# Optimization experiments

Hardware: AMD Instinct MI355X
Metric: run time of the kernel (lower is better)

## Reference

```python
import jax, jax.numpy as jnp
import numpy as np

# ---- config (matches init_kwargs) ----
B, C_IN, L, T = 32, 12, 1024, 64
C1, C2, K = 64, 128, 7
PAD = K // 2
NUM_CLASSES = 4
GAIN = 2.0
TH1, TH2 = 0.5, 0.5
TAU1, TAU2 = 1.0, 0.9
RESET = 0.0


def setup_inputs() -> dict:
    key = jax.random.key(0)
    ks = jax.random.split(key, 7)
    x = jax.random.normal(ks[0], (B, C_IN, L, T), dtype=jnp.float32)
    w1 = jax.random.normal(ks[1], (C1, C_IN, K), dtype=jnp.float32) * 0.1
    b1 = jax.random.normal(ks[2], (C1,), dtype=jnp.float32) * 0.01
    w2 = jax.random.normal(ks[3], (C2, C1, K), dtype=jnp.float32) * 0.05
    b2 = jax.random.normal(ks[4], (C2,), dtype=jnp.float32) * 0.01
    fc_w = jax.random.normal(ks[5], (NUM_CLASSES, C2), dtype=jnp.float32) * 0.1
    fc_b = jax.random.normal(ks[6], (NUM_CLASSES,), dtype=jnp.float32) * 0.01
    return {"x": x, "w1": w1, "b1": b1, "w2": w2, "b2": b2, "fc_w": fc_w, "fc_b": fc_b}


def _conv1d(x, w, b):
    # x: [B, Cin, L], w: [Cout, Cin, K] -> [B, Cout, L] (same padding)
    y = jax.lax.conv_general_dilated(
        x, w, window_strides=(1,), padding=[(PAD, PAD)],
        dimension_numbers=("NCW", "OIW", "NCW"))
    return y + b[None, :, None]


def _lif(v, inp, tau, thresh):
    # v <- v + (inp - v)/tau; spike = (v >= thresh); reset spiked neurons
    v = v + (inp - v) / tau
    spike = (v >= thresh).astype(inp.dtype)
    v = jnp.where(spike > 0, jnp.asarray(RESET, inp.dtype), v)
    return v, spike


def reference(x, w1, b1, w2, b2, fc_w, fc_b):
    # QuantStub/DeQuantStub are identity in the fp32 eager model.
    xs = jnp.transpose(x, (3, 0, 1, 2))  # [T, B, C_IN, L]

    def step(carry, xt):
        v1, v2, acc = carry
        h1 = _conv1d(xt, w1, b1) * GAIN
        v1, s1 = _lif(v1, h1, TAU1, TH1)
        h2 = _conv1d(s1, w2, b2) * GAIN
        v2, s2 = _lif(v2, h2, TAU2, TH2)
        return (v1, v2, acc + s2), None

    v1_0 = jnp.zeros((B, C1, L), x.dtype)
    v2_0 = jnp.zeros((B, C2, L), x.dtype)
    acc0 = jnp.zeros((B, C2, L), x.dtype)
    (_, _, acc), _ = jax.lax.scan(step, (v1_0, v2_0, acc0), xs)

    out = acc / jnp.asarray(T, x.dtype)          # [B, C2, L]
    out = jnp.mean(out, axis=-1)                  # AdaptiveAvgPool1d(1) + squeeze
    return out @ fc_w.T + fc_b                    # [B, NUM_CLASSES]
```

## Files before the change

### kernel.cpp

```cpp
#include <hip/hip_runtime.h>
#include <hip/hip_bf16.h>
#include <cstdint>

#define B_   32
#define CIN  12
#define L_   1024
#define T_   64
#define C1_  64
#define C2_  128
#define K_   7
#define PAD_ 3

typedef __attribute__((ext_vector_type(8))) short short8;
typedef __attribute__((ext_vector_type(4))) float float4v;

#define WS_S1T   0ull
#define WS_W2HI  268435456ull
#define WS_W1F   (WS_W2HI + 114688ull)
#define WS_POOL  (WS_W1F + 32768ull)

static __device__ __forceinline__ ushort bf16_hi(float f) {
    __hip_bfloat16 h = __float2bfloat16(f);
    ushort u; __builtin_memcpy(&u, &h, 2); return u;
}
static __device__ __forceinline__ float bf16_back(ushort u) {
    __hip_bfloat16 h; __builtin_memcpy(&h, &u, 2); return __bfloat162float(h);
}

__global__ __launch_bounds__(256) void k0_prep_w2(const float* __restrict__ w2,
                                                  ushort* __restrict__ w2hi,
                                                  float* __restrict__ pool) {
    int i = blockIdx.x * 256 + threadIdx.x;
    if (i < B_ * C2_) pool[i] = 0.0f;
    if (i >= C2_ * K_ * C1_) return;
    int c2 = i / (K_ * C1_);
    int r_ = i % (K_ * C1_);
    int kk = r_ / C1_;
    int c1 = r_ % C1_;
    float w = w2[(c2 * C1_ + c1) * K_ + kk];
    ushort uh = bf16_hi(w);
    int h    = c1 >> 5;
    int c1r  = c1 & 31;
    int e    = c1r >> 4;
    int kq   = (c1r >> 2) & 3;
    int rr   = c1r & 3;
    int j    = e * 4 + rr;
    int mt   = c2 >> 4;
    int lane = kq * 16 + (c2 & 15);
    int o    = ((((kk * 2 + h) * 8 + mt) * 64) + lane) * 8 + j;
    w2hi[o] = uh;
}

__global__ __launch_bounds__(256) void k0_prep_w1(const float* __restrict__ w1,
                                                  ushort* __restrict__ w1f) {
    int i = blockIdx.x * 256 + threadIdx.x;
    if (i >= 16384) return;
    int j    = i & 7;
    int lane = (i >> 3) & 63;
    int mf   = (i >> 9) & 3;
    int ks   = (i >> 11) & 3;
    int cp   = i >> 13;
    int k    = ks * 32 + (lane >> 4) * 8 + j;
    int dl   = k >> 4;
    int slot = k & 15;
    int c1   = mf * 16 + (lane & 15);
    float v  = (slot < CIN && dl < K_) ? w1[(c1 * CIN + slot) * K_ + dl] : 0.0f;
    ushort hi = bf16_hi(v);
    float  rem = v - bf16_back(hi);
    ushort lo = bf16_hi(rem);
    w1f[i] = cp ? lo : hi;
}

__global__ __launch_bounds__(256, 2) void k1_conv1_mfma(const float* __restrict__ x,
                                                        const ushort* __restrict__ w1f,
                                                        const float* __restrict__ b1,
                                                        ushort* __restrict__ s1t) {
    __shared__ __align__(16) ushort S[10 * 2048];
    int tid  = threadIdx.x;
    int lane = tid & 63;
    int wl   = tid >> 6;
    int b    = blockIdx.y;
    int bx   = blockIdx.x;
    int swz  = ((bx & 7) << 5) | (bx >> 3);
    int lb   = swz * 4;

    #pragma unroll
    for (int it = 0; it < 5; ++it) {
        int u  = it * 256 + tid;
        int t  = u & 63;
        int h2 = (u >> 6) & 1;
        int lp = u >> 7;
        int gl = lb + lp - PAD_;
        bool ok = (gl >= 0) && (gl < L_);
        short8 hv, lv;
        #pragma unroll
        for (int jj = 0; jj < 8; ++jj) {
            int cin = h2 * 8 + jj;
            float v = (ok && cin < CIN)
                ? x[(((size_t)b * CIN + cin) * L_ + gl) * T_ + t] : 0.0f;
            ushort hb = bf16_hi(v);
            ushort lo = bf16_hi(v - bf16_back(hb));
            hv[jj] = (short)hb;
            lv[jj] = (short)lo;
        }
        int nt = t >> 4, t15 = t & 15;
        int base = lp * 2048 + nt * 256 + h2 * 128 + t15 * 8;
        *(short8*)&S[base]        = hv;
        *(short8*)&S[base + 1024] = lv;
    }
    __syncthreads();

    int t15 = lane & 15;
    int h2l = (lane >> 4) & 1;
    int kqh = lane >> 5;

    float4v acc[4][4];
    #pragma unroll
    for (int i = 0; i < 4; ++i)
        #pragma unroll
        for (int jn = 0; jn < 4; ++jn)
            acc[i][jn] = (float4v){0.0f, 0.0f, 0.0f, 0.0f};

    #pragma unroll
    for (int ks = 0; ks < 4; ++ks) {
        int dtap = ks * 2 + kqh;
        int lpr  = (dtap == 7) ? 0 : (wl + dtap);
        int rb   = lpr * 2048 + h2l * 128 + t15 * 8;
        short8 bh[4], bl[4];
        #pragma unroll
        for (int nt = 0; nt < 4; ++nt) {
            bh[nt] = *(const short8*)&S[rb + nt * 256];
            bl[nt] = *(const short8*)&S[rb + nt * 256 + 1024];
        }
        #pragma unroll
        for (int mf = 0; mf < 4; ++mf) {
            const ushort* ap = w1f + ((size_t)(ks * 4 + mf) * 64 + lane) * 8;
            short8 ah = *(const short8*)ap;
            short8 al = *(const short8*)(ap + 8192);
            #pragma unroll
            for (int nt = 0; nt < 4; ++nt) {
                acc[mf][nt] = __builtin_amdgcn_mfma_f32_16x16x32_bf16(ah, bh[nt], acc[mf][nt], 0, 0, 0);
                acc[mf][nt] = __builtin_amdgcn_mfma_f32_16x16x32_bf16(al, bh[nt], acc[mf][nt], 0, 0, 0);
                acc[mf][nt] = __builtin_amdgcn_mfma_f32_16x16x32_bf16(ah, bl[nt], acc[mf][nt], 0, 0, 0);
            }
        }
    }

    int l  = lb + wl;
    int kq = lane >> 4;
    #pragma unroll
    for (int h = 0; h < 2; ++h) {
        float4v be0 = *(const float4v*)&b1[h * 32 + kq * 4];
        float4v be1 = *(const float4v*)&b1[h * 32 + 16 + kq * 4];
        #pragma unroll
        for (int nt = 0; nt < 4; ++nt) {
            uint s0 = (acc[2 * h][nt][0] + be0[0] >= 0.25f) ? 0x3F80u : 0u;
            uint s1 = (acc[2 * h][nt][1] + be0[1] >= 0.25f) ? 0x3F80u : 0u;
            uint s2 = (acc[2 * h][nt][2] + be0[2] >= 0.25f) ? 0x3F80u : 0u;
            uint s3 = (acc[2 * h][nt][3] + be0[3] >= 0.25f) ? 0x3F80u : 0u;
            uint s4 = (acc[2 * h + 1][nt][0] + be1[0] >= 0.25f) ? 0x3F80u : 0u;
            uint s5 = (acc[2 * h + 1][nt][1] + be1[1] >= 0.25f) ? 0x3F80u : 0u;
            uint s6 = (acc[2 * h + 1][nt][2] + be1[2] >= 0.25f) ? 0x3F80u : 0u;
            uint s7 = (acc[2 * h + 1][nt][3] + be1[3] >= 0.25f) ? 0x3F80u : 0u;
            uint4 u4 = { s0 | (s1 << 16), s2 | (s3 << 16),
                         s4 | (s5 << 16), s6 | (s7 << 16) };
            size_t off = ((((size_t)b * L_ + l) * 2 + h) * T_ + (nt * 16 + t15)) * 32 + kq * 8;
            *(uint4*)&s1t[off] = u4;
        }
    }
}

__global__ __launch_bounds__(512, 2) void k2_conv2_lif(const ushort* __restrict__ s1t,
                                                       const ushort* __restrict__ w2hi,
                                                       const float* __restrict__ b2,
                                                       float* __restrict__ pool) {
    __shared__ __align__(16) unsigned char lds_raw[40960];
    ushort* S = (ushort*)lds_raw;
    int tid    = threadIdx.x;
    int wv     = tid >> 6;
    int lane   = tid & 63;
    int wn     = wv >> 1;
    int wm     = wv & 1;
    int b      = blockIdx.y;
    int bx     = blockIdx.x;
    int swz    = ((bx & 7) << 5) | (bx >> 3);
    int lb     = swz * 4;
    int lane15 = lane & 15;
    int kq     = lane >> 4;

    float4v acc[4][4];
    #pragma unroll
    for (int i = 0; i < 4; ++i)
        #pragma unroll
        for (int j = 0; j < 4; ++j)
            acc[i][j] = (float4v){0.0f, 0.0f, 0.0f, 0.0f};

    #pragma unroll 1
    for (int h = 0; h < 2; ++h) {
        __syncthreads();
        #pragma unroll
        for (int it = 0; it < 2; ++it) {
            int u = it * 512 + tid;
            if (u < 640) {
                int lp = u >> 6, t = u & 63;
                int gl = lb + lp - PAD_;
                uint4 v0 = {0,0,0,0}, v1 = {0,0,0,0}, v2 = {0,0,0,0}, v3 = {0,0,0,0};
                if (gl >= 0 && gl < L_) {
                    const uint4* q = (const uint4*)&s1t[((((size_t)b * L_ + gl) * 2 + h) * T_) * 32 + (size_t)t * 32];
                    v0 = q[0]; v1 = q[1]; v2 = q[2]; v3 = q[3];
                }
                int nt = t >> 4, t15 = t & 15;
                int base = lp * 2048 + nt * 512 + t15 * 8;
                *(uint4*)&S[base]       = v0;
                *(uint4*)&S[base + 128] = v1;
                *(uint4*)&S[base + 256] = v2;
                *(uint4*)&S[base + 384] = v3;
            }
        }
        __syncthreads();
        #pragma unroll 2
        for (int kk = 0; kk < K_; ++kk) {
            int lp = wn + kk;
            short8 bf[4];
            #pragma unroll
            for (int nt = 0; nt < 4; ++nt)
                bf[nt] = *(const short8*)&S[lp * 2048 + nt * 512 + lane * 8];
            #pragma unroll
            for (int mf = 0; mf < 4; ++mf) {
                int aoff = (((kk * 2 + h) * 8 + wm * 4 + mf) * 64 + lane) * 8;
                short8 ahi = *(const short8*)&w2hi[aoff];
                #pragma unroll
                for (int nt = 0; nt < 4; ++nt)
                    acc[mf][nt] = __builtin_amdgcn_mfma_f32_16x16x32_bf16(ahi, bf[nt], acc[mf][nt], 0, 0, 0);
            }
        }
    }
    __syncthreads();

    float* E = ((float*)lds_raw) + wv * 1088;
    int c2v = wm * 64 + lane;
    const float Af = 1.0f - 1.0f / 0.9f;
    const float Cs = 2.0f / 0.9f;
    float D = b2[c2v] * Cs;
    float v = 0.0f;
    uint cnt = 0u;
    #pragma unroll
    for (int nt = 0; nt < 4; ++nt) {
        *(float4v*)&E[lane15 * 68 + 0 * 16 + kq * 4] = acc[0][nt];
        *(float4v*)&E[lane15 * 68 + 1 * 16 + kq * 4] = acc[1][nt];
        *(float4v*)&E[lane15 * 68 + 2 * 16 + kq * 4] = acc[2][nt];
        *(float4v*)&E[lane15 * 68 + 3 * 16 + kq * 4] = acc[3][nt];
        __builtin_amdgcn_s_waitcnt(0);
        #pragma unroll
        for (int tt = 0; tt < 16; ++tt) {
            float e = fmaf(E[tt * 68 + lane], Cs, D);
            v = fmaf(Af, v, e);
            bool sp = (v >= 0.5f);
            cnt += sp ? 1u : 0u;
            v = sp ? 0.0f : v;
        }
        __builtin_amdgcn_s_waitcnt(0);
    }
    atomicAdd(&pool[b * C2_ + c2v], (float)cnt);
}

__global__ __launch_bounds__(128) void k3_fc(const float* __restrict__ pool,
                                             const float* __restrict__ fcw,
                                             const float* __restrict__ fcb,
                                             float* __restrict__ out) {
    int i = threadIdx.x;
    int b = i >> 2, c = i & 3;
    float o = fcb[c];
    #pragma unroll 8
    for (int c2 = 0; c2 < C2_; ++c2)
        o = fmaf(fcw[c * C2_ + c2], pool[b * C2_ + c2] * (1.0f / 65536.0f), o);
    out[b * 4 + c] = o;
}

extern "C" void kernel_launch(void* const* d_in, const int* in_sizes, int n_in,
                              void* d_out, int out_size, void* d_ws, size_t ws_size,
                              hipStream_t stream) {
    const float* x   = (const float*)d_in[0];
    const float* w1  = (const float*)d_in[1];
    const float* b1  = (const float*)d_in[2];
    const float* w2  = (const float*)d_in[3];
    const float* b2  = (const float*)d_in[4];
    const float* fcw = (const float*)d_in[5];
    const float* fcb = (const float*)d_in[6];
    float* out = (float*)d_out;

    char* ws = (char*)d_ws;
    ushort* s1t  = (ushort*)(ws + WS_S1T);
    ushort* w2h  = (ushort*)(ws + WS_W2HI);
    ushort* w1f  = (ushort*)(ws + WS_W1F);
    float*  pool = (float*)(ws + WS_POOL);

    k0_prep_w2<<<dim3((C2_ * K_ * C1_ + 255) / 256), dim3(256), 0, stream>>>(w2, w2h, pool);
    k0_prep_w1<<<dim3(64), dim3(256), 0, stream>>>(w1, w1f);
    k1_conv1_mfma<<<dim3(L_ / 4, B_), dim3(256), 0, stream>>>(x, w1f, b1, s1t);
    k2_conv2_lif<<<dim3(L_ / 4, B_), dim3(512), 0, stream>>>(s1t, w2h, b2, pool);
    k3_fc<<<dim3(1), dim3(128), 0, stream>>>(pool, fcw, fcb, out);
}
```

Before: 524.9 us.

## Widen conv1 tiles to 8 positions and stage conv2 input via global_load_lds

Conv1 now runs 512-thread blocks covering 8 sequence positions instead of 4. This cuts the halo overhead of reloading and splitting x into bf16 hi/lo per block from 10/4 to 14/8, at the cost of more LDS per block. Conv2 stages its spike tiles with direct global-to-LDS loads (global_load_lds) instead of loading into registers and then storing to LDS. Out-of-range halo rows read from a zeroed scratch buffer that the prep kernel initialises.

```diff
diff --git a/kernel.cpp b/kernel.cpp
--- a/kernel.cpp
+++ b/kernel.cpp
@@ -18,6 +18,12 @@
 #define WS_W2HI  268435456ull
 #define WS_W1F   (WS_W2HI + 114688ull)
 #define WS_POOL  (WS_W1F + 32768ull)
+#define WS_ZP    (WS_POOL + 16384ull)
+
+#define GLOAD_LDS(SRC, DST)                                                        \
+    __builtin_amdgcn_global_load_lds(                                              \
+        (const __attribute__((address_space(1))) unsigned int*)(const void*)(SRC), \
+        (__attribute__((address_space(3))) unsigned int*)(void*)(DST), 16, 0, 0)
 
 static __device__ __forceinline__ ushort bf16_hi(float f) {
     __hip_bfloat16 h = __float2bfloat16(f);
@@ -29,9 +35,11 @@
 
 __global__ __launch_bounds__(256) void k0_prep_w2(const float* __restrict__ w2,
                                                   ushort* __restrict__ w2hi,
-                                                  float* __restrict__ pool) {
+                                                  float* __restrict__ pool,
+                                                  ushort* __restrict__ zp) {
     int i = blockIdx.x * 256 + threadIdx.x;
     if (i < B_ * C2_) pool[i] = 0.0f;
+    if (i < 2048) zp[i] = 0;
     if (i >= C2_ * K_ * C1_) return;
     int c2 = i / (K_ * C1_);
     int r_ = i % (K_ * C1_);
@@ -71,42 +79,44 @@
     w1f[i] = cp ? lo : hi;
 }
 
-__global__ __launch_bounds__(256, 2) void k1_conv1_mfma(const float* __restrict__ x,
+__global__ __launch_bounds__(512, 4) void k1_conv1_mfma(const float* __restrict__ x,
                                                         const ushort* __restrict__ w1f,
                                                         const float* __restrict__ b1,
                                                         ushort* __restrict__ s1t) {
-    __shared__ __align__(16) ushort S[10 * 2048];
+    __shared__ __align__(16) ushort S[14 * 2048];
     int tid  = threadIdx.x;
     int lane = tid & 63;
     int wl   = tid >> 6;
     int b    = blockIdx.y;
     int bx   = blockIdx.x;
-    int swz  = ((bx & 7) << 5) | (bx >> 3);
-    int lb   = swz * 4;
-
-    #pragma unroll
-    for (int it = 0; it < 5; ++it) {
-        int u  = it * 256 + tid;
-        int t  = u & 63;
-        int h2 = (u >> 6) & 1;
-        int lp = u >> 7;
-        int gl = lb + lp - PAD_;
-        bool ok = (gl >= 0) && (gl < L_);
-        short8 hv, lv;
-        #pragma unroll
-        for (int jj = 0; jj < 8; ++jj) {
-            int cin = h2 * 8 + jj;
-            float v = (ok && cin < CIN)
-                ? x[(((size_t)b * CIN + cin) * L_ + gl) * T_ + t] : 0.0f;
-            ushort hb = bf16_hi(v);
-            ushort lo = bf16_hi(v - bf16_back(hb));
-            hv[jj] = (short)hb;
-            lv[jj] = (short)lo;
-        }
-        int nt = t >> 4, t15 = t & 15;
-        int base = lp * 2048 + nt * 256 + h2 * 128 + t15 * 8;
-        *(short8*)&S[base]        = hv;
-        *(short8*)&S[base + 1024] = lv;
+    int swz  = ((bx & 7) << 4) | (bx >> 3);
+    int lb   = swz * 8;
+
+    #pragma unroll
+    for (int it = 0; it < 4; ++it) {
+        int u = it * 512 + tid;
+        if (u < 1792) {
+            int t  = u & 63;
+            int h2 = (u >> 6) & 1;
+            int lp = u >> 7;
+            int gl = lb + lp - PAD_;
+            bool ok = (gl >= 0) && (gl < L_);
+            short8 hv, lv;
+            #pragma unroll
+            for (int jj = 0; jj < 8; ++jj) {
+                int cin = h2 * 8 + jj;
+                float v = (ok && cin < CIN)
+                    ? x[(((size_t)b * CIN + cin) * L_ + gl) * T_ + t] : 0.0f;
+                ushort hb = bf16_hi(v);
+                ushort lo = bf16_hi(v - bf16_back(hb));
+                hv[jj] = (short)hb;
+                lv[jj] = (short)lo;
+            }
+            int nt = t >> 4, t15 = t & 15;
+            int base = lp * 2048 + nt * 256 + h2 * 128 + t15 * 8;
+            *(short8*)&S[base]        = hv;
+            *(short8*)&S[base + 1024] = lv;
+        }
     }
     __syncthreads();
 
@@ -173,7 +183,8 @@
 __global__ __launch_bounds__(512, 2) void k2_conv2_lif(const ushort* __restrict__ s1t,
                                                        const ushort* __restrict__ w2hi,
                                                        const float* __restrict__ b2,
-                                                       float* __restrict__ pool) {
+                                                       float* __restrict__ pool,
+                                                       const ushort* __restrict__ zp) {
     __shared__ __align__(16) unsigned char lds_raw[40960];
     ushort* S = (ushort*)lds_raw;
     int tid    = threadIdx.x;
@@ -187,6 +198,7 @@
     int lb     = swz * 4;
     int lane15 = lane & 15;
     int kq     = lane >> 4;
+    int srcoff = lane15 * 32 + (lane >> 4) * 8;
 
     float4v acc[4][4];
     #pragma unroll
@@ -199,22 +211,18 @@
     for (int h = 0; h < 2; ++h) {
         __syncthreads();
         #pragma unroll
-        for (int it = 0; it < 2; ++it) {
-            int u = it * 512 + tid;
-            if (u < 640) {
-                int lp = u >> 6, t = u & 63;
-                int gl = lb + lp - PAD_;
-                uint4 v0 = {0,0,0,0}, v1 = {0,0,0,0}, v2 = {0,0,0,0}, v3 = {0,0,0,0};
-                if (gl >= 0 && gl < L_) {
-                    const uint4* q = (const uint4*)&s1t[((((size_t)b * L_ + gl) * 2 + h) * T_) * 32 + (size_t)t * 32];
-                    v0 = q[0]; v1 = q[1]; v2 = q[2]; v3 = q[3];
-                }
-                int nt = t >> 4, t15 = t & 15;
-                int base = lp * 2048 + nt * 512 + t15 * 8;
-                *(uint4*)&S[base]       = v0;
-                *(uint4*)&S[base + 128] = v1;
-                *(uint4*)&S[base + 256] = v2;
-                *(uint4*)&S[base + 384] = v3;
+        for (int r0 = 0; r0 < 2; ++r0) {
+            int r = r0 * 8 + wv;
+            if (r < 10) {
+                int gl = lb + r - PAD_;
+                const ushort* srow = (gl >= 0 && gl < L_)
+                    ? &s1t[(((size_t)b * L_ + gl) * 2 + h) * 2048] : zp;
+                const ushort* s = srow + srcoff;
+                ushort* d = &S[r * 2048];
+                GLOAD_LDS(s,        d);
+                GLOAD_LDS(s + 512,  d + 512);
+                GLOAD_LDS(s + 1024, d + 1024);
+                GLOAD_LDS(s + 1536, d + 1536);
             }
         }
         __syncthreads();
@@ -294,10 +302,11 @@
     ushort* w2h  = (ushort*)(ws + WS_W2HI);
     ushort* w1f  = (ushort*)(ws + WS_W1F);
     float*  pool = (float*)(ws + WS_POOL);
-
-    k0_prep_w2<<<dim3((C2_ * K_ * C1_ + 255) / 256), dim3(256), 0, stream>>>(w2, w2h, pool);
+    ushort* zp   = (ushort*)(ws + WS_ZP);
+
+    k0_prep_w2<<<dim3((C2_ * K_ * C1_ + 255) / 256), dim3(256), 0, stream>>>(w2, w2h, pool, zp);
     k0_prep_w1<<<dim3(64), dim3(256), 0, stream>>>(w1, w1f);
-    k1_conv1_mfma<<<dim3(L_ / 4, B_), dim3(256), 0, stream>>>(x, w1f, b1, s1t);
-    k2_conv2_lif<<<dim3(L_ / 4, B_), dim3(512), 0, stream>>>(s1t, w2h, b2, pool);
+    k1_conv1_mfma<<<dim3(L_ / 8, B_), dim3(512), 0, stream>>>(x, w1f, b1, s1t);
+    k2_conv2_lif<<<dim3(L_ / 4, B_), dim3(512), 0, stream>>>(s1t, w2h, b2, pool, zp);
     k3_fc<<<dim3(1), dim3(128), 0, stream>>>(pool, fcw, fcb, out);
 }
```

Measured after the change: 553.6 us. 5.5% more time.

## Bit-pack conv1 spikes into uint words and expand to bf16 in conv2 LDS

Applied to the files above, without the earlier changes.

The conv1 spike tensor goes from a bf16 intermediate (one 16-bit value per spike) to one bit per spike, packed into 32-bit words. Conv2 expands each byte back into bf16 1.0/0.0 values while filling shared memory. This cuts the intermediate from 256MB to 16MB of global traffic at the cost of extra ALU work for packing and unpacking. The change also merges the two weight-prep kernels into one launch and raises the conv1 occupancy hint to 3 blocks per CU.

```diff
diff --git a/kernel.cpp b/kernel.cpp
--- a/kernel.cpp
+++ b/kernel.cpp
@@ -14,8 +14,8 @@
 typedef __attribute__((ext_vector_type(8))) short short8;
 typedef __attribute__((ext_vector_type(4))) float float4v;
 
-#define WS_S1T   0ull
-#define WS_W2HI  268435456ull
+#define WS_S1B   0ull
+#define WS_W2HI  16777216ull
 #define WS_W1F   (WS_W2HI + 114688ull)
 #define WS_POOL  (WS_W1F + 32768ull)
 
@@ -27,11 +27,38 @@
     __hip_bfloat16 h; __builtin_memcpy(&h, &u, 2); return __bfloat162float(h);
 }
 
-__global__ __launch_bounds__(256) void k0_prep_w2(const float* __restrict__ w2,
-                                                  ushort* __restrict__ w2hi,
-                                                  float* __restrict__ pool) {
+static __device__ __forceinline__ uint4 expand_byte(uint byte) {
+    uint4 e;
+    e.x = ((byte & 1u)   ? 0x3F80u : 0u) | ((byte & 2u)   ? 0x3F800000u : 0u);
+    e.y = ((byte & 4u)   ? 0x3F80u : 0u) | ((byte & 8u)   ? 0x3F800000u : 0u);
+    e.z = ((byte & 16u)  ? 0x3F80u : 0u) | ((byte & 32u)  ? 0x3F800000u : 0u);
+    e.w = ((byte & 64u)  ? 0x3F80u : 0u) | ((byte & 128u) ? 0x3F800000u : 0u);
+    return e;
+}
+
+__global__ __launch_bounds__(256) void k0_prep(const float* __restrict__ w2,
+                                               ushort* __restrict__ w2hi,
+                                               const float* __restrict__ w1,
+                                               ushort* __restrict__ w1f,
+                                               float* __restrict__ pool) {
     int i = blockIdx.x * 256 + threadIdx.x;
     if (i < B_ * C2_) pool[i] = 0.0f;
+    if (i < 16384) {
+        int j    = i & 7;
+        int lane = (i >> 3) & 63;
+        int mf   = (i >> 9) & 3;
+        int ks   = (i >> 11) & 3;
+        int cp   = i >> 13;
+        int k    = ks * 32 + (lane >> 4) * 8 + j;
+        int dl   = k >> 4;
+        int slot = k & 15;
+        int c1   = mf * 16 + (lane & 15);
+        float v  = (slot < CIN && dl < K_) ? w1[(c1 * CIN + slot) * K_ + dl] : 0.0f;
+        ushort hi = bf16_hi(v);
+        float  rem = v - bf16_back(hi);
+        ushort lo = bf16_hi(rem);
+        w1f[i] = cp ? lo : hi;
+    }
     if (i >= C2_ * K_ * C1_) return;
     int c2 = i / (K_ * C1_);
     int r_ = i % (K_ * C1_);
@@ -51,30 +78,10 @@
     w2hi[o] = uh;
 }
 
-__global__ __launch_bounds__(256) void k0_prep_w1(const float* __restrict__ w1,
-                                                  ushort* __restrict__ w1f) {
-    int i = blockIdx.x * 256 + threadIdx.x;
-    if (i >= 16384) return;
-    int j    = i & 7;
-    int lane = (i >> 3) & 63;
-    int mf   = (i >> 9) & 3;
-    int ks   = (i >> 11) & 3;
-    int cp   = i >> 13;
-    int k    = ks * 32 + (lane >> 4) * 8 + j;
-    int dl   = k >> 4;
-    int slot = k & 15;
-    int c1   = mf * 16 + (lane & 15);
-    float v  = (slot < CIN && dl < K_) ? w1[(c1 * CIN + slot) * K_ + dl] : 0.0f;
-    ushort hi = bf16_hi(v);
-    float  rem = v - bf16_back(hi);
-    ushort lo = bf16_hi(rem);
-    w1f[i] = cp ? lo : hi;
-}
-
-__global__ __launch_bounds__(256, 2) void k1_conv1_mfma(const float* __restrict__ x,
+__global__ __launch_bounds__(256, 3) void k1_conv1_mfma(const float* __restrict__ x,
                                                         const ushort* __restrict__ w1f,
                                                         const float* __restrict__ b1,
-                                                        ushort* __restrict__ s1t) {
+                                                        uint* __restrict__ s1b) {
     __shared__ __align__(16) ushort S[10 * 2048];
     int tid  = threadIdx.x;
     int lane = tid & 63;
@@ -152,25 +159,25 @@
     for (int h = 0; h < 2; ++h) {
         float4v be0 = *(const float4v*)&b1[h * 32 + kq * 4];
         float4v be1 = *(const float4v*)&b1[h * 32 + 16 + kq * 4];
+        uint w = 0u;
         #pragma unroll
         for (int nt = 0; nt < 4; ++nt) {
-            uint s0 = (acc[2 * h][nt][0] + be0[0] >= 0.25f) ? 0x3F80u : 0u;
-            uint s1 = (acc[2 * h][nt][1] + be0[1] >= 0.25f) ? 0x3F80u : 0u;
-            uint s2 = (acc[2 * h][nt][2] + be0[2] >= 0.25f) ? 0x3F80u : 0u;
-            uint s3 = (acc[2 * h][nt][3] + be0[3] >= 0.25f) ? 0x3F80u : 0u;
-            uint s4 = (acc[2 * h + 1][nt][0] + be1[0] >= 0.25f) ? 0x3F80u : 0u;
-            uint s5 = (acc[2 * h + 1][nt][1] + be1[1] >= 0.25f) ? 0x3F80u : 0u;
-            uint s6 = (acc[2 * h + 1][nt][2] + be1[2] >= 0.25f) ? 0x3F80u : 0u;
-            uint s7 = (acc[2 * h + 1][nt][3] + be1[3] >= 0.25f) ? 0x3F80u : 0u;
-            uint4 u4 = { s0 | (s1 << 16), s2 | (s3 << 16),
-                         s4 | (s5 << 16), s6 | (s7 << 16) };
-            size_t off = ((((size_t)b * L_ + l) * 2 + h) * T_ + (nt * 16 + t15)) * 32 + kq * 8;
-            *(uint4*)&s1t[off] = u4;
-        }
-    }
-}
-
-__global__ __launch_bounds__(512, 2) void k2_conv2_lif(const ushort* __restrict__ s1t,
+            uint byte =
+                ((acc[2 * h][nt][0]     + be0[0] >= 0.25f) ? 1u   : 0u) |
+                ((acc[2 * h][nt][1]     + be0[1] >= 0.25f) ? 2u   : 0u) |
+                ((acc[2 * h][nt][2]     + be0[2] >= 0.25f) ? 4u   : 0u) |
+                ((acc[2 * h][nt][3]     + be0[3] >= 0.25f) ? 8u   : 0u) |
+                ((acc[2 * h + 1][nt][0] + be1[0] >= 0.25f) ? 16u  : 0u) |
+                ((acc[2 * h + 1][nt][1] + be1[1] >= 0.25f) ? 32u  : 0u) |
+                ((acc[2 * h + 1][nt][2] + be1[2] >= 0.25f) ? 64u  : 0u) |
+                ((acc[2 * h + 1][nt][3] + be1[3] >= 0.25f) ? 128u : 0u);
+            w |= byte << (8 * nt);
+        }
+        s1b[((size_t)(b * L_ + l) * 2 + h) * 64 + t15 * 4 + kq] = w;
+    }
+}
+
+__global__ __launch_bounds__(512, 2) void k2_conv2_lif(const uint* __restrict__ s1b,
                                                        const ushort* __restrict__ w2hi,
                                                        const float* __restrict__ b2,
                                                        float* __restrict__ pool) {
@@ -202,19 +209,16 @@
         for (int it = 0; it < 2; ++it) {
             int u = it * 512 + tid;
             if (u < 640) {
-                int lp = u >> 6, t = u & 63;
+                int lp = u >> 6, w = u & 63;
                 int gl = lb + lp - PAD_;
-                uint4 v0 = {0,0,0,0}, v1 = {0,0,0,0}, v2 = {0,0,0,0}, v3 = {0,0,0,0};
-                if (gl >= 0 && gl < L_) {
-                    const uint4* q = (const uint4*)&s1t[((((size_t)b * L_ + gl) * 2 + h) * T_) * 32 + (size_t)t * 32];
-                    v0 = q[0]; v1 = q[1]; v2 = q[2]; v3 = q[3];
-                }
-                int nt = t >> 4, t15 = t & 15;
-                int base = lp * 2048 + nt * 512 + t15 * 8;
-                *(uint4*)&S[base]       = v0;
-                *(uint4*)&S[base + 128] = v1;
-                *(uint4*)&S[base + 256] = v2;
-                *(uint4*)&S[base + 384] = v3;
+                uint bits = (gl >= 0 && gl < L_)
+                    ? s1b[((size_t)(b * L_ + gl) * 2 + h) * 64 + w] : 0u;
+                int st15 = w >> 2, skq = w & 3;
+                int base = lp * 2048 + skq * 128 + st15 * 8;
+                *(uint4*)&S[base]        = expand_byte(bits & 0xffu);
+                *(uint4*)&S[base + 512]  = expand_byte((bits >> 8) & 0xffu);
+                *(uint4*)&S[base + 1024] = expand_byte((bits >> 16) & 0xffu);
+                *(uint4*)&S[base + 1536] = expand_byte(bits >> 24);
             }
         }
         __syncthreads();
@@ -290,14 +294,13 @@
     float* out = (float*)d_out;
 
     char* ws = (char*)d_ws;
-    ushort* s1t  = (ushort*)(ws + WS_S1T);
+    uint*   s1b  = (uint*)(ws + WS_S1B);
     ushort* w2h  = (ushort*)(ws + WS_W2HI);
     ushort* w1f  = (ushort*)(ws + WS_W1F);
     float*  pool = (float*)(ws + WS_POOL);
 
-    k0_prep_w2<<<dim3((C2_ * K_ * C1_ + 255) / 256), dim3(256), 0, stream>>>(w2, w2h, pool);
-    k0_prep_w1<<<dim3(64), dim3(256), 0, stream>>>(w1, w1f);
-    k1_conv1_mfma<<<dim3(L_ / 4, B_), dim3(256), 0, stream>>>(x, w1f, b1, s1t);
-    k2_conv2_lif<<<dim3(L_ / 4, B_), dim3(512), 0, stream>>>(s1t, w2h, b2, pool);
+    k0_prep<<<dim3((C2_ * K_ * C1_ + 255) / 256), dim3(256), 0, stream>>>(w2, w2h, w1, w1f, pool);
+    k1_conv1_mfma<<<dim3(L_ / 4, B_), dim3(256), 0, stream>>>(x, w1f, b1, s1b);
+    k2_conv2_lif<<<dim3(L_ / 4, B_), dim3(512), 0, stream>>>(s1b, w2h, b2, pool);
     k3_fc<<<dim3(1), dim3(128), 0, stream>>>(pool, fcw, fcb, out);
 }
```

Result: faster. 483.5 us (-7.9%).
